# Optimization experiments

Measured on AMD Instinct MI355X. Metric: run time of the kernel, lower is better.

## Reference

```python
import jax, jax.numpy as jnp
import numpy as np

B, N, C, F, O = 32, 2048, 8, 128, 128


def setup_inputs() -> dict:
    key = jax.random.key(0)
    k1, k2, k3, k4, k5, k6 = jax.random.split(key, 6)
    nodes = jax.random.normal(k1, (B, N, F), dtype=jnp.float32)
    children = jax.random.randint(k2, (B, N, C), 0, N, dtype=jnp.int32)
    w_t = jax.random.normal(k3, (F, O), dtype=jnp.float32) * 0.05
    w_l = jax.random.normal(k4, (F, O), dtype=jnp.float32) * 0.05
    w_r = jax.random.normal(k5, (F, O), dtype=jnp.float32) * 0.05
    b = jax.random.normal(k6, (O,), dtype=jnp.float32) * 0.05
    return {"nodes": nodes, "children": children, "w_t": w_t, "w_l": w_l, "w_r": w_r, "b": b}


def reference(nodes, children, w_t, w_l, w_r, b):
    Bb, Nn, Ff = nodes.shape
    Cc = children.shape[2]
    dt = nodes.dtype

    # --- children tensor: index 0 maps to zero vector ---
    lookup = jnp.concatenate([jnp.zeros((Bb, 1, Ff), dt), nodes[:, 1:, :]], axis=1)
    batch_idx = jnp.arange(Bb)[:, None, None]
    child_vecs = lookup[batch_idx, children]                      # [B,N,C,F]
    tree = jnp.concatenate([nodes[:, :, None, :], child_vecs], axis=2)  # [B,N,C+1,F]

    # --- coefficients ---
    ch_f = children.astype(dt)
    c_t = jnp.broadcast_to(
        jnp.concatenate([jnp.ones((1, 1, 1), dt), jnp.zeros((1, 1, Cc), dt)], axis=2),
        (Bb, Nn, Cc + 1))                                          # [B,N,C+1]
    num_sib = jnp.count_nonzero(children, axis=2, keepdims=True).astype(dt)  # [B,N,1]
    mask = jnp.concatenate(
        [jnp.zeros((Bb, Nn, 1), dt), jnp.minimum(ch_f, 1.0)], axis=2)        # [B,N,C+1]
    child_indices = jnp.arange(-1.0, Cc, 1.0, dtype=dt)[None, None, :] * mask
    singles = jnp.concatenate(
        [jnp.zeros((Bb, Nn, 1), dt),
         jnp.full((Bb, Nn, 1), 0.5, dt),
         jnp.zeros((Bb, Nn, Cc - 1), dt)], axis=2)
    is_single = num_sib == 1.0
    denom = jnp.where(is_single, 1.0, num_sib - 1.0)  # safe divide, matches tf.where select
    c_r = jnp.where(is_single, singles, (1.0 - c_t) * (child_indices / denom))
    c_l = (1.0 - c_t) * (1.0 - c_r) * mask
    coef = jnp.stack([c_t, c_r, c_l], axis=3)                      # [B,N,C+1,3]

    # --- weighted aggregation + small GEMM ---
    agg = jnp.einsum('bncf,bnck->bnkf', tree, coef)                # [B,N,3,F]
    w = jnp.stack([w_t, w_r, w_l], axis=0)                         # [3,F,O]
    out = jnp.einsum('bnkf,kfo->bno', agg, w)
    return jax.nn.relu(out + b)
```

## Files before the change

### kernel.cpp

```cpp
#include <hip/hip_runtime.h>

typedef unsigned short ushort_t;
typedef __attribute__((ext_vector_type(8))) short short8;
typedef __attribute__((ext_vector_type(4))) short short4v;
typedef __attribute__((ext_vector_type(4))) float float4v;

#define Bn 32
#define Nn 2048
#define Cn 8
#define Fn 128
#define On 128
#define Kn 384
#define MT 32
#define LDSK 392

__device__ __forceinline__ ushort_t f2bf(float x) {
  unsigned u = __float_as_uint(x);
  u += 0x7fffu + ((u >> 16) & 1u);
  return (ushort_t)(u >> 16);
}

__global__ void prep_w_kernel(const float* __restrict__ w_t,
                              const float* __restrict__ w_l,
                              const float* __restrict__ w_r,
                              ushort_t* __restrict__ wcT) {
  int i = blockIdx.x * blockDim.x + threadIdx.x;
  if (i >= On * Kn) return;
  int o = i / Kn;
  int k = i - o * Kn;
  const float* src = (k < Fn) ? w_t : (k < 2 * Fn) ? w_r : w_l;
  int f = k & (Fn - 1);
  wcT[i] = f2bf(src[f * On + o]);
}

__global__ __launch_bounds__(256)
void tree_conv_kernel(const float* __restrict__ nodes,
                      const int* __restrict__ children,
                      const ushort_t* __restrict__ wcT,
                      const float* __restrict__ bias,
                      float* __restrict__ out) {
  __shared__ __align__(16) ushort_t agg[MT * LDSK];

  const int tid = threadIdx.x;

  const int sb = ((blockIdx.x & 7) << 8) | (blockIdx.x >> 3);

  {
    const int row = tid >> 3;
    const int fc = (tid & 7) * 16;
    const int g = sb * MT + row;
    const int base_row = g & ~(Nn - 1);

    const int4* chv = (const int4*)(children + g * Cn);
    int4 ca = chv[0], cb = chv[1];
    int idx[Cn] = {ca.x, ca.y, ca.z, ca.w, cb.x, cb.y, cb.z, cb.w};

    int ns = 0;
#pragma unroll
    for (int c = 0; c < Cn; ++c) ns += (idx[c] != 0);
    const float denom = (ns > 1) ? (float)(ns - 1) : 1.0f;

    float crv[Cn], clv[Cn];
#pragma unroll
    for (int c = 0; c < Cn; ++c) {
      float m = (idx[c] != 0) ? 1.0f : 0.0f;
      float cr0 = (ns == 1) ? ((c == 0) ? 0.5f : 0.0f) : ((float)c / denom);
      float cr = cr0 * m;
      crv[c] = cr;
      clv[c] = (1.0f - cr) * m;
    }

    ushort_t* arow = agg + row * LDSK;

    const float4v* sp = (const float4v*)(nodes + (size_t)g * Fn + fc);
    float4v s0 = sp[0], s1 = sp[1], s2 = sp[2], s3 = sp[3];
    {
      short8 pk0 = {(short)f2bf(s0.x), (short)f2bf(s0.y), (short)f2bf(s0.z), (short)f2bf(s0.w),
                    (short)f2bf(s1.x), (short)f2bf(s1.y), (short)f2bf(s1.z), (short)f2bf(s1.w)};
      short8 pk1 = {(short)f2bf(s2.x), (short)f2bf(s2.y), (short)f2bf(s2.z), (short)f2bf(s2.w),
                    (short)f2bf(s3.x), (short)f2bf(s3.y), (short)f2bf(s3.z), (short)f2bf(s3.w)};
      *(short8*)(arow + fc) = pk0;
      *(short8*)(arow + fc + 8) = pk1;
    }

    float4v r[4], l[4];
    const float4v z = {0.f, 0.f, 0.f, 0.f};
#pragma unroll
    for (int j = 0; j < 4; ++j) { r[j] = z; l[j] = z; }

#pragma unroll
    for (int c = 0; c < Cn; ++c) {
      const float4v* cp =
          (const float4v*)(nodes + (size_t)(base_row + idx[c]) * Fn + fc);
      const float cr = crv[c], cl = clv[c];
#pragma unroll
      for (int j = 0; j < 4; ++j) {
        float4v v = cp[j];
        r[j] += cr * v;
        l[j] += cl * v;
      }
    }

    {
      short8 pk0 = {(short)f2bf(r[0].x), (short)f2bf(r[0].y), (short)f2bf(r[0].z), (short)f2bf(r[0].w),
                    (short)f2bf(r[1].x), (short)f2bf(r[1].y), (short)f2bf(r[1].z), (short)f2bf(r[1].w)};
      short8 pk1 = {(short)f2bf(r[2].x), (short)f2bf(r[2].y), (short)f2bf(r[2].z), (short)f2bf(r[2].w),
                    (short)f2bf(r[3].x), (short)f2bf(r[3].y), (short)f2bf(r[3].z), (short)f2bf(r[3].w)};
      *(short8*)(arow + Fn + fc) = pk0;
      *(short8*)(arow + Fn + fc + 8) = pk1;
      short8 pk2 = {(short)f2bf(l[0].x), (short)f2bf(l[0].y), (short)f2bf(l[0].z), (short)f2bf(l[0].w),
                    (short)f2bf(l[1].x), (short)f2bf(l[1].y), (short)f2bf(l[1].z), (short)f2bf(l[1].w)};
      short8 pk3 = {(short)f2bf(l[2].x), (short)f2bf(l[2].y), (short)f2bf(l[2].z), (short)f2bf(l[2].w),
                    (short)f2bf(l[3].x), (short)f2bf(l[3].y), (short)f2bf(l[3].z), (short)f2bf(l[3].w)};
      *(short8*)(arow + 2 * Fn + fc) = pk2;
      *(short8*)(arow + 2 * Fn + fc + 8) = pk3;
    }
  }

  const int lane = tid & 63;
  const int wave = tid >> 6;
  const int l15 = lane & 15;
  const int quad = lane >> 4;

  short8 bfrag[2][12];
#pragma unroll
  for (int ct = 0; ct < 2; ++ct) {
    const ushort_t* bp = wcT + (size_t)(wave * 32 + ct * 16 + l15) * Kn + quad * 8;
#pragma unroll
    for (int ks = 0; ks < 12; ++ks)
      bfrag[ct][ks] = *(const short8*)(bp + ks * 32);
  }

  const float bias0 = bias[wave * 32 + l15];
  const float bias1 = bias[wave * 32 + 16 + l15];

  __syncthreads();

#pragma unroll 1
  for (int st = 0; st < 2; ++st) {
    const ushort_t* ar = agg + (st * 16 + l15) * LDSK + quad * 8;
    float4v acc0 = {0.f, 0.f, 0.f, 0.f};
    float4v acc1 = {0.f, 0.f, 0.f, 0.f};
#pragma unroll
    for (int ks = 0; ks < 12; ++ks) {
      short8 af = *(const short8*)(ar + ks * 32);
      acc0 = __builtin_amdgcn_mfma_f32_16x16x32_bf16(af, bfrag[0][ks], acc0, 0, 0, 0);
      acc1 = __builtin_amdgcn_mfma_f32_16x16x32_bf16(af, bfrag[1][ks], acc1, 0, 0, 0);
    }
    const int grow0 = sb * MT + st * 16 + quad * 4;
    const int col0 = wave * 32 + l15;
#pragma unroll
    for (int r2 = 0; r2 < 4; ++r2) {
      float v0 = acc0[r2] + bias0;
      float v1 = acc1[r2] + bias1;
      out[(size_t)(grow0 + r2) * On + col0] = fmaxf(v0, 0.f);
      out[(size_t)(grow0 + r2) * On + col0 + 16] = fmaxf(v1, 0.f);
    }
  }
}

extern "C" void kernel_launch(void* const* d_in, const int* in_sizes, int n_in,
                              void* d_out, int out_size, void* d_ws, size_t ws_size,
                              hipStream_t stream) {
  const float* nodes = (const float*)d_in[0];
  const int* children = (const int*)d_in[1];
  const float* w_t = (const float*)d_in[2];
  const float* w_l = (const float*)d_in[3];
  const float* w_r = (const float*)d_in[4];
  const float* bias = (const float*)d_in[5];
  float* out = (float*)d_out;
  ushort_t* wcT = (ushort_t*)d_ws;

  prep_w_kernel<<<(On * Kn + 255) / 256, 256, 0, stream>>>(w_t, w_l, w_r, wcT);
  tree_conv_kernel<<<(Bn * Nn) / MT, 256, 0, stream>>>(nodes, children, wcT, bias, out);
}
```

Measured before the change: 135.6 us.

## Coalesce gathers per row, pre-swizzle weight fragments, reduce MFMA register footprint

The gather phase now uses 32 lanes per row, each loading one float4. A single child row is therefore read as one contiguous 512-byte access instead of 16-float chunks spread over 8 threads, and each thread processes 4 rows in sequence. The weights are pre-swizzled into MFMA fragment order so each lane reads them with fully coalesced short8 loads. The MFMA loop now handles one column tile at a time, which halves the B-fragment registers held and may improve occupancy. The trade-off is more serial work per thread in the gather and one MFMA accumulator chain instead of two interleaved chains.

```diff
diff --git a/kernel.cpp b/kernel.cpp
--- a/kernel.cpp
+++ b/kernel.cpp
@@ -23,20 +23,31 @@
 __global__ void prep_w_kernel(const float* __restrict__ w_t,
                               const float* __restrict__ w_l,
                               const float* __restrict__ w_r,
-                              ushort_t* __restrict__ wcT) {
-  int i = blockIdx.x * blockDim.x + threadIdx.x;
-  if (i >= On * Kn) return;
-  int o = i / Kn;
-  int k = i - o * Kn;
-  const float* src = (k < Fn) ? w_t : (k < 2 * Fn) ? w_r : w_l;
-  int f = k & (Fn - 1);
-  wcT[i] = f2bf(src[f * On + o]);
+                              ushort_t* __restrict__ wsw) {
+  int t = blockIdx.x * blockDim.x + threadIdx.x;
+  if (t >= 6144) return;
+  int lane = t & 63;
+  int r = t >> 6;
+  int ks = r % 12;
+  int q = r / 12;
+  int ct = q & 1;
+  int w = q >> 1;
+  int col = w * 32 + ct * 16 + (lane & 15);
+  int kbase = ((lane >> 4) * 8) + ks * 32;
+  ushort_t* dst = wsw + (size_t)t * 8;
+#pragma unroll
+  for (int j = 0; j < 8; ++j) {
+    int k = kbase + j;
+    const float* src = (k < Fn) ? w_t : (k < 2 * Fn) ? w_r : w_l;
+    int f = k & (Fn - 1);
+    dst[j] = f2bf(src[f * On + col]);
+  }
 }
 
 __global__ __launch_bounds__(256)
 void tree_conv_kernel(const float* __restrict__ nodes,
                       const int* __restrict__ children,
-                      const ushort_t* __restrict__ wcT,
+                      const ushort_t* __restrict__ wsw,
                       const float* __restrict__ bias,
                       float* __restrict__ out) {
   __shared__ __align__(16) ushort_t agg[MT * LDSK];
@@ -46,115 +57,91 @@
   const int sb = ((blockIdx.x & 7) << 8) | (blockIdx.x >> 3);
 
   {
-    const int row = tid >> 3;
-    const int fc = (tid & 7) * 16;
-    const int g = sb * MT + row;
-    const int base_row = g & ~(Nn - 1);
-
-    const int4* chv = (const int4*)(children + g * Cn);
-    int4 ca = chv[0], cb = chv[1];
-    int idx[Cn] = {ca.x, ca.y, ca.z, ca.w, cb.x, cb.y, cb.z, cb.w};
-
-    int ns = 0;
-#pragma unroll
-    for (int c = 0; c < Cn; ++c) ns += (idx[c] != 0);
-    const float denom = (ns > 1) ? (float)(ns - 1) : 1.0f;
-
-    float crv[Cn], clv[Cn];
-#pragma unroll
-    for (int c = 0; c < Cn; ++c) {
-      float m = (idx[c] != 0) ? 1.0f : 0.0f;
-      float cr0 = (ns == 1) ? ((c == 0) ? 0.5f : 0.0f) : ((float)c / denom);
-      float cr = cr0 * m;
-      crv[c] = cr;
-      clv[c] = (1.0f - cr) * m;
-    }
-
-    ushort_t* arow = agg + row * LDSK;
-
-    const float4v* sp = (const float4v*)(nodes + (size_t)g * Fn + fc);
-    float4v s0 = sp[0], s1 = sp[1], s2 = sp[2], s3 = sp[3];
-    {
-      short8 pk0 = {(short)f2bf(s0.x), (short)f2bf(s0.y), (short)f2bf(s0.z), (short)f2bf(s0.w),
-                    (short)f2bf(s1.x), (short)f2bf(s1.y), (short)f2bf(s1.z), (short)f2bf(s1.w)};
-      short8 pk1 = {(short)f2bf(s2.x), (short)f2bf(s2.y), (short)f2bf(s2.z), (short)f2bf(s2.w),
-                    (short)f2bf(s3.x), (short)f2bf(s3.y), (short)f2bf(s3.z), (short)f2bf(s3.w)};
-      *(short8*)(arow + fc) = pk0;
-      *(short8*)(arow + fc + 8) = pk1;
-    }
-
-    float4v r[4], l[4];
-    const float4v z = {0.f, 0.f, 0.f, 0.f};
-#pragma unroll
-    for (int j = 0; j < 4; ++j) { r[j] = z; l[j] = z; }
+    const int grp = tid >> 5;
+    const int ln = tid & 31;
 
 #pragma unroll
-    for (int c = 0; c < Cn; ++c) {
-      const float4v* cp =
-          (const float4v*)(nodes + (size_t)(base_row + idx[c]) * Fn + fc);
-      const float cr = crv[c], cl = clv[c];
+    for (int it = 0; it < 4; ++it) {
+      const int row = it * 8 + grp;
+      const int g = sb * MT + row;
+      const int base_row = g & ~(Nn - 1);
+
+      const int4* chv = (const int4*)(children + (size_t)g * Cn);
+      int4 ca = chv[0], cb = chv[1];
+      int idx[Cn] = {ca.x, ca.y, ca.z, ca.w, cb.x, cb.y, cb.z, cb.w};
+
+      int ns = 0;
 #pragma unroll
-      for (int j = 0; j < 4; ++j) {
-        float4v v = cp[j];
-        r[j] += cr * v;
-        l[j] += cl * v;
+      for (int c = 0; c < Cn; ++c) ns += (idx[c] != 0);
+      const float denom = (ns > 1) ? (float)(ns - 1) : 1.0f;
+
+      float crv[Cn], clv[Cn];
+#pragma unroll
+      for (int c = 0; c < Cn; ++c) {
+        float m = (idx[c] != 0) ? 1.0f : 0.0f;
+        float cr0 = (ns == 1) ? ((c == 0) ? 0.5f : 0.0f) : ((float)c / denom);
+        float cr = cr0 * m;
+        crv[c] = cr;
+        clv[c] = (1.0f - cr) * m;
+        idx[c] &= (Nn - 1);
       }
-    }
 
-    {
-      short8 pk0 = {(short)f2bf(r[0].x), (short)f2bf(r[0].y), (short)f2bf(r[0].z), (short)f2bf(r[0].w),
-                    (short)f2bf(r[1].x), (short)f2bf(r[1].y), (short)f2bf(r[1].z), (short)f2bf(r[1].w)};
-      short8 pk1 = {(short)f2bf(r[2].x), (short)f2bf(r[2].y), (short)f2bf(r[2].z), (short)f2bf(r[2].w),
-                    (short)f2bf(r[3].x), (short)f2bf(r[3].y), (short)f2bf(r[3].z), (short)f2bf(r[3].w)};
-      *(short8*)(arow + Fn + fc) = pk0;
-      *(short8*)(arow + Fn + fc + 8) = pk1;
-      short8 pk2 = {(short)f2bf(l[0].x), (short)f2bf(l[0].y), (short)f2bf(l[0].z), (short)f2bf(l[0].w),
-                    (short)f2bf(l[1].x), (short)f2bf(l[1].y), (short)f2bf(l[1].z), (short)f2bf(l[1].w)};
-      short8 pk3 = {(short)f2bf(l[2].x), (short)f2bf(l[2].y), (short)f2bf(l[2].z), (short)f2bf(l[2].w),
-                    (short)f2bf(l[3].x), (short)f2bf(l[3].y), (short)f2bf(l[3].z), (short)f2bf(l[3].w)};
-      *(short8*)(arow + 2 * Fn + fc) = pk2;
-      *(short8*)(arow + 2 * Fn + fc + 8) = pk3;
+      const float4v sv = *((const float4v*)(nodes + (size_t)g * Fn) + ln);
+
+      float4v rr = {0.f, 0.f, 0.f, 0.f};
+      float4v ll = {0.f, 0.f, 0.f, 0.f};
+#pragma unroll
+      for (int c = 0; c < Cn; ++c) {
+        const float4v v =
+            *((const float4v*)(nodes + (size_t)(base_row + idx[c]) * Fn) + ln);
+        rr += crv[c] * v;
+        ll += clv[c] * v;
+      }
+
+      ushort_t* arow = agg + row * LDSK;
+      short4v ps = {(short)f2bf(sv.x), (short)f2bf(sv.y),
+                    (short)f2bf(sv.z), (short)f2bf(sv.w)};
+      short4v pr = {(short)f2bf(rr.x), (short)f2bf(rr.y),
+                    (short)f2bf(rr.z), (short)f2bf(rr.w)};
+      short4v pl = {(short)f2bf(ll.x), (short)f2bf(ll.y),
+                    (short)f2bf(ll.z), (short)f2bf(ll.w)};
+      *(short4v*)(arow + ln * 4) = ps;
+      *(short4v*)(arow + Fn + ln * 4) = pr;
+      *(short4v*)(arow + 2 * Fn + ln * 4) = pl;
     }
   }
+
+  __syncthreads();
 
   const int lane = tid & 63;
   const int wave = tid >> 6;
   const int l15 = lane & 15;
   const int quad = lane >> 4;
 
-  short8 bfrag[2][12];
 #pragma unroll
   for (int ct = 0; ct < 2; ++ct) {
-    const ushort_t* bp = wcT + (size_t)(wave * 32 + ct * 16 + l15) * Kn + quad * 8;
+    const short8* bp = (const short8*)wsw + ((wave * 2 + ct) * 12) * 64 + lane;
+    short8 bfrag[12];
 #pragma unroll
-    for (int ks = 0; ks < 12; ++ks)
-      bfrag[ct][ks] = *(const short8*)(bp + ks * 32);
-  }
+    for (int ks = 0; ks < 12; ++ks) bfrag[ks] = bp[ks * 64];
 
-  const float bias0 = bias[wave * 32 + l15];
-  const float bias1 = bias[wave * 32 + 16 + l15];
+    const int col = wave * 32 + ct * 16 + l15;
+    const float bb = bias[col];
 
-  __syncthreads();
-
-#pragma unroll 1
-  for (int st = 0; st < 2; ++st) {
-    const ushort_t* ar = agg + (st * 16 + l15) * LDSK + quad * 8;
-    float4v acc0 = {0.f, 0.f, 0.f, 0.f};
-    float4v acc1 = {0.f, 0.f, 0.f, 0.f};
 #pragma unroll
-    for (int ks = 0; ks < 12; ++ks) {
-      short8 af = *(const short8*)(ar + ks * 32);
-      acc0 = __builtin_amdgcn_mfma_f32_16x16x32_bf16(af, bfrag[0][ks], acc0, 0, 0, 0);
-      acc1 = __builtin_amdgcn_mfma_f32_16x16x32_bf16(af, bfrag[1][ks], acc1, 0, 0, 0);
-    }
-    const int grow0 = sb * MT + st * 16 + quad * 4;
-    const int col0 = wave * 32 + l15;
+    for (int st = 0; st < 2; ++st) {
+      const ushort_t* ar = agg + (st * 16 + l15) * LDSK + quad * 8;
+      float4v acc = {0.f, 0.f, 0.f, 0.f};
 #pragma unroll
-    for (int r2 = 0; r2 < 4; ++r2) {
-      float v0 = acc0[r2] + bias0;
-      float v1 = acc1[r2] + bias1;
-      out[(size_t)(grow0 + r2) * On + col0] = fmaxf(v0, 0.f);
-      out[(size_t)(grow0 + r2) * On + col0 + 16] = fmaxf(v1, 0.f);
+      for (int ks = 0; ks < 12; ++ks) {
+        short8 af = *(const short8*)(ar + ks * 32);
+        acc = __builtin_amdgcn_mfma_f32_16x16x32_bf16(af, bfrag[ks], acc, 0, 0, 0);
+      }
+      const int grow0 = sb * MT + st * 16 + quad * 4;
+#pragma unroll
+      for (int r2 = 0; r2 < 4; ++r2) {
+        out[(size_t)(grow0 + r2) * On + col] = fmaxf(acc[r2] + bb, 0.f);
+      }
     }
   }
 }
@@ -169,8 +156,8 @@
   const float* w_r = (const float*)d_in[4];
   const float* bias = (const float*)d_in[5];
   float* out = (float*)d_out;
-  ushort_t* wcT = (ushort_t*)d_ws;
+  ushort_t* wsw = (ushort_t*)d_ws;
 
-  prep_w_kernel<<<(On * Kn + 255) / 256, 256, 0, stream>>>(w_t, w_l, w_r, wcT);
-  tree_conv_kernel<<<(Bn * Nn) / MT, 256, 0, stream>>>(nodes, children, wcT, bias, out);
+  prep_w_kernel<<<24, 256, 0, stream>>>(w_t, w_l, w_r, wsw);
+  tree_conv_kernel<<<(Bn * Nn) / MT, 256, 0, stream>>>(nodes, children, wsw, bias, out);
 }
```

Result: faster. 122.9 us (-9.4%).
